# Kernel tuning notes

Hardware: AMD Instinct MI355X
Metric: run time of the kernel (lower is better)

Reference implementation:

```python
import jax, jax.numpy as jnp
import numpy as np
from jax import lax

K, N, DV, NBPS, NITER, BATCH = 1056, 2112, 5, 4, 20, 1024
M = N - K            # number of parity checks
E = M * (DV + 1)     # Tanner-graph edges (H = [A | I_m], row weight DV+1)
NSYM = N // NBPS     # QAM symbols per codeword


def _qam16():
    # Sionna-style Gray-mapped QAM constellation, unit average energy.
    def pam_gray(b):
        if len(b) > 1:
            return (1 - 2 * b[0]) * (2 ** (len(b) - 1) - pam_gray(b[1:]))
        return 1 - 2 * b[0]
    pts = []
    for i in range(2 ** NBPS):
        b = [(i >> (NBPS - 1 - j)) & 1 for j in range(NBPS)]
        pts.append(complex(pam_gray(b[0::2]), pam_gray(b[1::2])))
    pts = np.asarray(pts)
    pts = pts / np.sqrt(np.mean(np.abs(pts) ** 2))
    return pts.real.astype(np.float32), pts.imag.astype(np.float32)


def setup_inputs() -> dict:
    key = jax.random.key(0)
    rng = np.random.default_rng(0)
    bits = jnp.asarray(rng.integers(0, 2, size=(BATCH, K)), jnp.int32)
    # sparse A: DV distinct info-bit columns per check row
    a_idx = np.argsort(rng.random((M, K)), axis=1)[:, :DV].astype(np.int32)
    edge_vn = np.concatenate([a_idx, K + np.arange(M, dtype=np.int32)[:, None]], axis=1).reshape(-1)
    edge_cn = np.repeat(np.arange(M, dtype=np.int32), DV + 1)
    pre, pim = _qam16()
    k1, k2 = jax.random.split(key)
    return {
        "bits": bits,
        "a_idx": jnp.asarray(a_idx),
        "edge_cn": jnp.asarray(edge_cn),
        "edge_vn": jnp.asarray(edge_vn),
        "points_re": jnp.asarray(pre),
        "points_im": jnp.asarray(pim),
        "noise_re": jax.random.normal(k1, (BATCH, NSYM), jnp.float32),
        "noise_im": jax.random.normal(k2, (BATCH, NSYM), jnp.float32),
        "ebno_db": jnp.float32(4.0),
    }


def _forward(bits, a_idx, edge_cn, edge_vn, points_re, points_im, noise_re, noise_im, ebno_db):
    B = bits.shape[0]
    coderate = K / N
    # ebnodb2no (Es = 1): N0 = 1 / (EbN0_lin * coderate * bits_per_symbol)
    no = 1.0 / (10.0 ** (ebno_db / 10.0) * coderate * NBPS)
    # --- LDPC encode: H = [A | I], parity_i = XOR of info bits in row i ---
    parity = jnp.sum(bits[:, a_idx], axis=-1) % 2          # [B, M]
    cw = jnp.concatenate([bits, parity], axis=1)           # [B, N]
    # --- QAM map ---
    w = jnp.array([1 << (NBPS - 1 - j) for j in range(NBPS)], jnp.int32)
    sym = jnp.sum(cw.reshape(B, NSYM, NBPS) * w, axis=-1)  # [B, S]
    sigma = jnp.sqrt(no / 2.0)
    y_re = points_re[sym] + sigma * noise_re
    y_im = points_im[sym] + sigma * noise_im
    # --- APP demap: LLR = log p(b=0|y) - log p(b=1|y) ---
    d2 = (y_re[..., None] - points_re) ** 2 + (y_im[..., None] - points_im) ** 2  # [B,S,16]
    lg = (-d2 / no)[..., None]                                                     # [B,S,16,1]
    lab = (jnp.arange(2 ** NBPS)[:, None] >> jnp.arange(NBPS - 1, -1, -1)) & 1     # [16,4]
    NEG = jnp.float32(-1e30)
    l0 = jax.nn.logsumexp(jnp.where(lab == 0, lg, NEG), axis=2)
    l1 = jax.nn.logsumexp(jnp.where(lab == 1, lg, NEG), axis=2)
    llr = (l0 - l1).reshape(B, N)                          # [B, N]
    # --- sum-product BP, flooding schedule, NITER iterations ---
    def marg(c2v):  # scatter-add check->variable messages onto variable nodes
        return jnp.zeros((B, N), c2v.dtype).at[:, edge_vn].add(c2v)
    def step(c2v, _):
        v2c = (llr + marg(c2v))[:, edge_vn] - c2v          # extrinsic VN->CN [B,E]
        av = jnp.clip(jnp.abs(v2c), 1e-6, 20.0)
        lt = jnp.log(jnp.tanh(av * 0.5))                   # log|tanh(.)| <= 0
        sg = (v2c < 0).astype(v2c.dtype)
        cs = jnp.zeros((B, M), v2c.dtype).at[:, edge_cn].add(lt)
        ns = jnp.zeros((B, M), v2c.dtype).at[:, edge_cn].add(sg)
        ex = jnp.exp(jnp.minimum(cs[:, edge_cn] - lt, -1e-7))   # prod over other edges < 1
        sp = 1.0 - 2.0 * jnp.mod(ns[:, edge_cn] - sg, 2.0)      # sign product over other edges
        return sp * 2.0 * jnp.arctanh(ex), None
    c2v, _ = lax.scan(step, jnp.zeros((B, E), jnp.float32), None, length=NITER)
    tot = llr + marg(c2v)
    bits_rx = (tot[:, :K] < 0).astype(jnp.float32)         # hard_out=True
    return bits.astype(jnp.float32), bits_rx, tot[:, :K]


def reference(bits, a_idx, edge_cn, edge_vn, points_re, points_im, noise_re, noise_im, ebno_db):
    b, brx, _ = _forward(bits, a_idx, edge_cn, edge_vn, points_re, points_im,
                         noise_re, noise_im, ebno_db)
    return b, brx
```

## Files before the change

### kernel.cpp

```cpp
#include <hip/hip_runtime.h>

#define K_     1056
#define N_     2112
#define M_     1056
#define E_     6336
#define NIE_   5280
#define CAP_   6336
#define ALL_   7392
#define DV_    5
#define ROW_   6
#define NSYM_  528
#define NITER_ 20
#define BATCH_ 1024
#define BS_    1024
#define KMAX_  2

#define LOG2E_ 1.4426950408889634f
#define AVLO_  (1e-6f * LOG2E_)
#define AVHI_  (20.0f * LOG2E_)
#define QC_    0.99999988f

__device__ __forceinline__ int seg_stride(int d) { return d | 1; }

__device__ __forceinline__ float fexp2(float x) { return __builtin_amdgcn_exp2f(x); }
__device__ __forceinline__ float flog2(float x) { return __builtin_amdgcn_logf(x); }
__device__ __forceinline__ float frcp(float x)  { return __builtin_amdgcn_rcpf(x); }

__global__ __launch_bounds__(BS_, 8) void link_kernel(
    const int*   __restrict__ bits,
    const int*   __restrict__ a_idx,
    const float* __restrict__ points_re,
    const float* __restrict__ points_im,
    const float* __restrict__ noise_re,
    const float* __restrict__ noise_im,
    const float* __restrict__ ebno_db,
    const int*   __restrict__ edge_vn,
    float*       __restrict__ out)
{
#pragma clang fp contract(off)
    const int b   = blockIdx.x;
    const int tid = threadIdx.x;

    __shared__ float s_all[ALL_];
    __shared__ float s_pre[16];
    __shared__ float s_pim[16];
    __shared__ int   s_hist[32];
    __shared__ int   s_binStart[32];
    __shared__ int   s_binBase[32];

    float* s_mem  = s_all;
    float* s_marg = s_all + CAP_;

    int* sc        = (int*)(s_all + N_);
    int* s_deg     = sc;
    int* s_perm    = sc + K_;
    int* s_offslot = sc + 2 * K_;
    int* s_cnt     = sc + 3 * K_;

    if (tid < 16) {
        s_pre[tid] = points_re[tid];
        s_pim[tid] = points_im[tid];
    }
    if (tid < 32) s_hist[tid] = 0;

    const float eb    = ebno_db[0];
    const float no    = 1.0f / ((powf(10.0f, eb / 10.0f) * 0.5f) * 4.0f);
    const float sigma = sqrtf(no / 2.0f);

    for (int i = tid; i < K_; i += BS_) {
        int v = bits[b * K_ + i];
        s_mem[i] = (float)v;
        out[b * K_ + i] = (float)v;
    }
    __syncthreads();

    for (int m = tid; m < M_; m += BS_) {
        float acc = 0.0f;
        #pragma unroll
        for (int d = 0; d < DV_; ++d) acc += s_mem[a_idx[m * DV_ + d]];
        s_mem[K_ + m] = (float)(((int)acc) & 1);
    }
    for (int v = tid; v < K_; v += BS_) { s_deg[v] = 0; s_cnt[v] = 0; }
    __syncthreads();

    for (int s = tid; s < NSYM_; s += BS_) {
        int c0 = (int)s_mem[4 * s + 0];
        int c1 = (int)s_mem[4 * s + 1];
        int c2 = (int)s_mem[4 * s + 2];
        int c3 = (int)s_mem[4 * s + 3];
        int sym = c0 * 8 + c1 * 4 + c2 * 2 + c3;
        float yre = s_pre[sym] + sigma * noise_re[b * NSYM_ + s];
        float yim = s_pim[sym] + sigma * noise_im[b * NSYM_ + s];
        #pragma unroll
        for (int j = 0; j < 4; ++j) {
            float m0 = -1e30f, m1 = -1e30f;
            #pragma unroll
            for (int p = 0; p < 16; ++p) {
                float dre  = yre - s_pre[p];
                float dim_ = yim - s_pim[p];
                float lg   = -(dre * dre + dim_ * dim_) / no;
                if (((p >> (3 - j)) & 1) == 0) m0 = fmaxf(m0, lg);
                else                           m1 = fmaxf(m1, lg);
            }
            float sum0 = 0.0f, sum1 = 0.0f;
            #pragma unroll
            for (int p = 0; p < 16; ++p) {
                float dre  = yre - s_pre[p];
                float dim_ = yim - s_pim[p];
                float lg   = -(dre * dre + dim_ * dim_) / no;
                if (((p >> (3 - j)) & 1) == 0) sum0 += __expf(lg - m0);
                else                           sum1 += __expf(lg - m1);
            }
            float llr = (m0 + __logf(sum0)) - (m1 + __logf(sum1));
            s_mem[4 * s + j] = llr * LOG2E_;
        }
    }
    for (int idx = tid; idx < NIE_; idx += BS_) {
        int m = idx / 5, j = idx - m * 5;
        atomicAdd(&s_deg[edge_vn[m * ROW_ + j]], 1);
    }
    __syncthreads();

    for (int v = tid; v < K_; v += BS_) atomicAdd(&s_hist[s_deg[v] & 31], 1);
    __syncthreads();
    if (tid == 0) {
        int accS = 0, accB = 0;
        for (int d = 0; d < 32; ++d) {
            int c = s_hist[d];
            s_binStart[d] = accS;
            s_binBase[d]  = accB;
            s_hist[d]     = accS;
            accS += c;
            accB += c * seg_stride(d);
        }
    }
    __syncthreads();
    for (int v = tid; v < K_; v += BS_) {
        int d    = s_deg[v];
        int slot = atomicAdd(&s_hist[d & 31], 1);
        int base = s_binBase[d] + (slot - s_binStart[d]) * seg_stride(d);
        s_perm[slot]  = v | (d << 16);
        s_offslot[v]  = base | (slot << 16);
    }
    __syncthreads();

    int      pv[KMAX_];
    unsigned od[KMAX_];
    float    lr[KMAX_];
    #pragma unroll
    for (int k = 0; k < KMAX_; ++k) {
        int s = tid + BS_ * k;
        if (s < K_) {
            int w = s_perm[s];
            int v = w & 0xFFFF;
            int d = w >> 16;
            int base = s_binBase[d] + (s - s_binStart[d]) * seg_stride(d);
            pv[k] = v;
            od[k] = (unsigned)base | ((unsigned)d << 16);
            lr[k] = s_mem[v];
            s_marg[s] = lr[k];
        } else { pv[k] = 0; od[k] = 0; lr[k] = 0.0f; }
    }
    float    t5[KMAX_];
    unsigned vnp[KMAX_][5];
    float    c2v[KMAX_][5];
    #pragma unroll
    for (int kk = 0; kk < KMAX_; ++kk) {
        int m = tid + BS_ * kk;
        if (m < M_) {
            #pragma unroll
            for (int j = 0; j < 5; ++j) {
                int v = edge_vn[m * ROW_ + j];
                int r = atomicAdd(&s_cnt[v], 1);
                int w = s_offslot[v];
                int slot = w >> 16;
                int epos = (w & 0xFFFF) + r;
                vnp[kk][j] = (unsigned)(slot << 2) | ((unsigned)(epos << 2) << 16);
                c2v[kk][j] = 0.0f;
            }
            float lrP = s_mem[K_ + m];
            float av  = __builtin_amdgcn_fmed3f(fabsf(lrP), AVLO_, AVHI_);
            float e   = fexp2(-av);
            float tm  = (1.0f - e) * frcp(1.0f + e);
            t5[kk] = copysignf(tm, lrP);
        } else {
            t5[kk] = 0.0f;
            #pragma unroll
            for (int j = 0; j < 5; ++j) { vnp[kk][j] = 0; c2v[kk][j] = 0.0f; }
        }
    }
    __syncthreads();

    for (int it = 0; it < NITER_; ++it) {
        #pragma unroll
        for (int kk = 0; kk < KMAX_; ++kk) {
            int m = tid + BS_ * kk;
            if (m < M_) {
                float tj[5];
                #pragma unroll
                for (int j = 0; j < 5; ++j) {
                    unsigned w = vnp[kk][j];
                    float mgv = *(const float*)((const char*)s_all +
                                 ((w & 0xFFFFu) + (unsigned)(CAP_ * 4)));
                    float v2c = mgv - c2v[kk][j];
                    float av  = __builtin_amdgcn_fmed3f(fabsf(v2c), AVLO_, AVHI_);
                    float e   = fexp2(-av);
                    float tm  = (1.0f - e) * frcp(1.0f + e);
                    tj[j] = copysignf(tm, v2c);
                }
                float qv[5];
                float pr = t5[kk];
                #pragma unroll
                for (int j = 0; j < 5; ++j) { qv[j] = pr; pr *= tj[j]; }
                float sf = 1.0f;
                #pragma unroll
                for (int j = 4; j >= 0; --j) { qv[j] *= sf; sf *= tj[j]; }
                #pragma unroll
                for (int j = 0; j < 5; ++j) {
                    float q = __builtin_amdgcn_fmed3f(qv[j], -QC_, QC_);
                    float r = flog2((1.0f + q) * frcp(1.0f - q));
                    c2v[kk][j] = r;
                    *(float*)((char*)s_all + (vnp[kk][j] >> 16)) = r;
                }
            }
        }
        __syncthreads();
        #pragma unroll
        for (int k = 0; k < KMAX_; ++k) {
            int s = tid + BS_ * k;
            if (s < K_) {
                int base = (int)(od[k] & 0xFFFFu);
                int dg   = (int)(od[k] >> 16);
                float mg = lr[k];
                int d = 0;
                for (; d + 1 < dg; d += 2) {
                    mg += s_mem[base + d];
                    mg += s_mem[base + d + 1];
                }
                if (d < dg) mg += s_mem[base + d];
                s_marg[s] = mg;
                if (it == NITER_ - 1)
                    out[(size_t)BATCH_ * K_ + b * K_ + pv[k]] =
                        (mg < 0.0f) ? 1.0f : 0.0f;
            }
        }
        __syncthreads();
    }
}

extern "C" void kernel_launch(void* const* d_in, const int* in_sizes, int n_in,
                              void* d_out, int out_size, void* d_ws, size_t ws_size,
                              hipStream_t stream) {
    const int*   bits    = (const int*)  d_in[0];
    const int*   a_idx   = (const int*)  d_in[1];
    const int*   edge_vn = (const int*)  d_in[3];
    const float* pre     = (const float*)d_in[4];
    const float* pim     = (const float*)d_in[5];
    const float* nre     = (const float*)d_in[6];
    const float* nim     = (const float*)d_in[7];
    const float* ebno    = (const float*)d_in[8];

    link_kernel<<<BATCH_, BS_, 0, stream>>>(bits, a_idx, pre, pim, nre, nim,
                                            ebno, edge_vn, (float*)d_out);
}
```

Before: 181.5 us.

## Decode two codewords per block with interleaved float2 shared memory

Each block now processes two codewords. Messages and marginals are stored as interleaved float2 in shared memory, so the graph-structure setup (degree histogram, permutation, edge offsets) is amortized across both codewords and each LDS access moves 8 bytes. The grid is halved and shared memory usage doubles, which lowers occupancy and increases per-thread register pressure from the float2 arrays. An explicit zeroing pass over the message area is added before the iterations.

```diff
diff --git a/kernel.cpp b/kernel.cpp
--- a/kernel.cpp
+++ b/kernel.cpp
@@ -14,6 +14,7 @@
 #define BATCH_ 1024
 #define BS_    1024
 #define KMAX_  2
+#define NCW_   2
 
 #define LOG2E_ 1.4426950408889634f
 #define AVLO_  (1e-6f * LOG2E_)
@@ -38,20 +39,22 @@
     float*       __restrict__ out)
 {
 #pragma clang fp contract(off)
-    const int b   = blockIdx.x;
+    const int blk = blockIdx.x;
+    const int b0  = blk * NCW_;
+    const int b1  = b0 + 1;
     const int tid = threadIdx.x;
 
-    __shared__ float s_all[ALL_];
-    __shared__ float s_pre[16];
-    __shared__ float s_pim[16];
-    __shared__ int   s_hist[32];
-    __shared__ int   s_binStart[32];
-    __shared__ int   s_binBase[32];
-
-    float* s_mem  = s_all;
-    float* s_marg = s_all + CAP_;
-
-    int* sc        = (int*)(s_all + N_);
+    __shared__ float2 s_all2[ALL_];
+    __shared__ float  s_pre[16];
+    __shared__ float  s_pim[16];
+    __shared__ int    s_hist[32];
+    __shared__ int    s_binStart[32];
+    __shared__ int    s_binBase[32];
+
+    float* s_f = (float*)s_all2;
+    char*  sb  = (char*)s_all2;
+
+    int* sc        = (int*)(s_all2 + N_);
     int* s_deg     = sc;
     int* s_perm    = sc + K_;
     int* s_offslot = sc + 2 * K_;
@@ -68,29 +71,41 @@
     const float sigma = sqrtf(no / 2.0f);
 
     for (int i = tid; i < K_; i += BS_) {
-        int v = bits[b * K_ + i];
-        s_mem[i] = (float)v;
-        out[b * K_ + i] = (float)v;
+        int v0 = bits[b0 * K_ + i];
+        int v1 = bits[b1 * K_ + i];
+        s_f[2 * i + 0] = (float)v0;
+        s_f[2 * i + 1] = (float)v1;
+        out[b0 * K_ + i] = (float)v0;
+        out[b1 * K_ + i] = (float)v1;
     }
     __syncthreads();
 
     for (int m = tid; m < M_; m += BS_) {
-        float acc = 0.0f;
+        float ax = 0.0f, ay = 0.0f;
         #pragma unroll
-        for (int d = 0; d < DV_; ++d) acc += s_mem[a_idx[m * DV_ + d]];
-        s_mem[K_ + m] = (float)(((int)acc) & 1);
+        for (int d = 0; d < DV_; ++d) {
+            float2 f = s_all2[a_idx[m * DV_ + d]];
+            ax += f.x; ay += f.y;
+        }
+        float2 p;
+        p.x = (float)(((int)ax) & 1);
+        p.y = (float)(((int)ay) & 1);
+        s_all2[K_ + m] = p;
     }
     for (int v = tid; v < K_; v += BS_) { s_deg[v] = 0; s_cnt[v] = 0; }
     __syncthreads();
 
-    for (int s = tid; s < NSYM_; s += BS_) {
-        int c0 = (int)s_mem[4 * s + 0];
-        int c1 = (int)s_mem[4 * s + 1];
-        int c2 = (int)s_mem[4 * s + 2];
-        int c3 = (int)s_mem[4 * s + 3];
+    for (int tsk = tid; tsk < NCW_ * NSYM_; tsk += BS_) {
+        int cw = (tsk >= NSYM_) ? 1 : 0;
+        int s  = tsk - cw * NSYM_;
+        int bcw = b0 + cw;
+        int c0 = (int)s_f[2 * (4 * s + 0) + cw];
+        int c1 = (int)s_f[2 * (4 * s + 1) + cw];
+        int c2 = (int)s_f[2 * (4 * s + 2) + cw];
+        int c3 = (int)s_f[2 * (4 * s + 3) + cw];
         int sym = c0 * 8 + c1 * 4 + c2 * 2 + c3;
-        float yre = s_pre[sym] + sigma * noise_re[b * NSYM_ + s];
-        float yim = s_pim[sym] + sigma * noise_im[b * NSYM_ + s];
+        float yre = s_pre[sym] + sigma * noise_re[bcw * NSYM_ + s];
+        float yim = s_pim[sym] + sigma * noise_im[bcw * NSYM_ + s];
         #pragma unroll
         for (int j = 0; j < 4; ++j) {
             float m0 = -1e30f, m1 = -1e30f;
@@ -112,7 +127,7 @@
                 else                           sum1 += __expf(lg - m1);
             }
             float llr = (m0 + __logf(sum0)) - (m1 + __logf(sum1));
-            s_mem[4 * s + j] = llr * LOG2E_;
+            s_f[2 * (4 * s + j) + cw] = llr * LOG2E_;
         }
     }
     for (int idx = tid; idx < NIE_; idx += BS_) {
@@ -144,9 +159,8 @@
     }
     __syncthreads();
 
-    int      pv[KMAX_];
     unsigned od[KMAX_];
-    float    lr[KMAX_];
+    float2   lr[KMAX_];
     #pragma unroll
     for (int k = 0; k < KMAX_; ++k) {
         int s = tid + BS_ * k;
@@ -155,15 +169,14 @@
             int v = w & 0xFFFF;
             int d = w >> 16;
             int base = s_binBase[d] + (s - s_binStart[d]) * seg_stride(d);
-            pv[k] = v;
-            od[k] = (unsigned)base | ((unsigned)d << 16);
-            lr[k] = s_mem[v];
-            s_marg[s] = lr[k];
-        } else { pv[k] = 0; od[k] = 0; lr[k] = 0.0f; }
-    }
-    float    t5[KMAX_];
+            od[k] = (unsigned)base | ((unsigned)d << 13) | ((unsigned)v << 18);
+            lr[k] = s_all2[v];
+            s_all2[CAP_ + s] = lr[k];
+        } else { od[k] = 0; lr[k] = make_float2(0.0f, 0.0f); }
+    }
+    float2   t5[KMAX_];
     unsigned vnp[KMAX_][5];
-    float    c2v[KMAX_][5];
+    float2   c2v[KMAX_][5];
     #pragma unroll
     for (int kk = 0; kk < KMAX_; ++kk) {
         int m = tid + BS_ * kk;
@@ -175,20 +188,26 @@
                 int w = s_offslot[v];
                 int slot = w >> 16;
                 int epos = (w & 0xFFFF) + r;
-                vnp[kk][j] = (unsigned)(slot << 2) | ((unsigned)(epos << 2) << 16);
-                c2v[kk][j] = 0.0f;
-            }
-            float lrP = s_mem[K_ + m];
-            float av  = __builtin_amdgcn_fmed3f(fabsf(lrP), AVLO_, AVHI_);
-            float e   = fexp2(-av);
-            float tm  = (1.0f - e) * frcp(1.0f + e);
-            t5[kk] = copysignf(tm, lrP);
+                vnp[kk][j] = (unsigned)(slot << 3) | ((unsigned)(epos << 3) << 16);
+                c2v[kk][j] = make_float2(0.0f, 0.0f);
+            }
+            float2 lrP = s_all2[K_ + m];
+            float avx = __builtin_amdgcn_fmed3f(fabsf(lrP.x), AVLO_, AVHI_);
+            float avy = __builtin_amdgcn_fmed3f(fabsf(lrP.y), AVLO_, AVHI_);
+            float ex  = fexp2(-avx), ey = fexp2(-avy);
+            float tmx = (1.0f - ex) * frcp(1.0f + ex);
+            float tmy = (1.0f - ey) * frcp(1.0f + ey);
+            t5[kk] = make_float2(copysignf(tmx, lrP.x), copysignf(tmy, lrP.y));
         } else {
-            t5[kk] = 0.0f;
+            t5[kk] = make_float2(0.0f, 0.0f);
             #pragma unroll
-            for (int j = 0; j < 5; ++j) { vnp[kk][j] = 0; c2v[kk][j] = 0.0f; }
-        }
-    }
+            for (int j = 0; j < 5; ++j) {
+                vnp[kk][j] = 0; c2v[kk][j] = make_float2(0.0f, 0.0f);
+            }
+        }
+    }
+    __syncthreads();
+    for (int i = tid; i < CAP_; i += BS_) s_all2[i] = make_float2(0.0f, 0.0f);
     __syncthreads();
 
     for (int it = 0; it < NITER_; ++it) {
@@ -196,31 +215,43 @@
         for (int kk = 0; kk < KMAX_; ++kk) {
             int m = tid + BS_ * kk;
             if (m < M_) {
-                float tj[5];
+                float tjx[5], tjy[5];
                 #pragma unroll
                 for (int j = 0; j < 5; ++j) {
                     unsigned w = vnp[kk][j];
-                    float mgv = *(const float*)((const char*)s_all +
-                                 ((w & 0xFFFFu) + (unsigned)(CAP_ * 4)));
-                    float v2c = mgv - c2v[kk][j];
-                    float av  = __builtin_amdgcn_fmed3f(fabsf(v2c), AVLO_, AVHI_);
-                    float e   = fexp2(-av);
-                    float tm  = (1.0f - e) * frcp(1.0f + e);
-                    tj[j] = copysignf(tm, v2c);
-                }
-                float qv[5];
-                float pr = t5[kk];
-                #pragma unroll
-                for (int j = 0; j < 5; ++j) { qv[j] = pr; pr *= tj[j]; }
-                float sf = 1.0f;
-                #pragma unroll
-                for (int j = 4; j >= 0; --j) { qv[j] *= sf; sf *= tj[j]; }
+                    float2 mgv = *(const float2*)(sb +
+                                 ((w & 0xFFFFu) + (unsigned)(CAP_ * 8)));
+                    float vx = mgv.x - c2v[kk][j].x;
+                    float vy = mgv.y - c2v[kk][j].y;
+                    float avx = __builtin_amdgcn_fmed3f(fabsf(vx), AVLO_, AVHI_);
+                    float avy = __builtin_amdgcn_fmed3f(fabsf(vy), AVLO_, AVHI_);
+                    float ex = fexp2(-avx), ey = fexp2(-avy);
+                    float tmx = (1.0f - ex) * frcp(1.0f + ex);
+                    float tmy = (1.0f - ey) * frcp(1.0f + ey);
+                    tjx[j] = copysignf(tmx, vx);
+                    tjy[j] = copysignf(tmy, vy);
+                }
+                float qx[5], qy[5];
+                float prx = t5[kk].x, pry = t5[kk].y;
                 #pragma unroll
                 for (int j = 0; j < 5; ++j) {
-                    float q = __builtin_amdgcn_fmed3f(qv[j], -QC_, QC_);
-                    float r = flog2((1.0f + q) * frcp(1.0f - q));
-                    c2v[kk][j] = r;
-                    *(float*)((char*)s_all + (vnp[kk][j] >> 16)) = r;
+                    qx[j] = prx; qy[j] = pry;
+                    prx *= tjx[j]; pry *= tjy[j];
+                }
+                float sfx = 1.0f, sfy = 1.0f;
+                #pragma unroll
+                for (int j = 4; j >= 0; --j) {
+                    qx[j] *= sfx; qy[j] *= sfy;
+                    sfx *= tjx[j]; sfy *= tjy[j];
+                }
+                #pragma unroll
+                for (int j = 0; j < 5; ++j) {
+                    float qcx = __builtin_amdgcn_fmed3f(qx[j], -QC_, QC_);
+                    float qcy = __builtin_amdgcn_fmed3f(qy[j], -QC_, QC_);
+                    float rx = flog2((1.0f + qcx) * frcp(1.0f - qcx));
+                    float ry = flog2((1.0f + qcy) * frcp(1.0f - qcy));
+                    c2v[kk][j] = make_float2(rx, ry);
+                    *(float2*)(sb + (vnp[kk][j] >> 16)) = c2v[kk][j];
                 }
             }
         }
@@ -229,19 +260,26 @@
         for (int k = 0; k < KMAX_; ++k) {
             int s = tid + BS_ * k;
             if (s < K_) {
-                int base = (int)(od[k] & 0xFFFFu);
-                int dg   = (int)(od[k] >> 16);
-                float mg = lr[k];
+                int base = (int)(od[k] & 0x1FFFu);
+                int dg   = (int)((od[k] >> 13) & 31u);
+                float mgx = lr[k].x, mgy = lr[k].y;
                 int d = 0;
                 for (; d + 1 < dg; d += 2) {
-                    mg += s_mem[base + d];
-                    mg += s_mem[base + d + 1];
-                }
-                if (d < dg) mg += s_mem[base + d];
-                s_marg[s] = mg;
-                if (it == NITER_ - 1)
-                    out[(size_t)BATCH_ * K_ + b * K_ + pv[k]] =
-                        (mg < 0.0f) ? 1.0f : 0.0f;
+                    float2 f0 = s_all2[base + d];
+                    float2 f1 = s_all2[base + d + 1];
+                    mgx += f0.x; mgy += f0.y;
+                    mgx += f1.x; mgy += f1.y;
+                }
+                if (d < dg) {
+                    float2 f0 = s_all2[base + d];
+                    mgx += f0.x; mgy += f0.y;
+                }
+                s_all2[CAP_ + s] = make_float2(mgx, mgy);
+                if (it == NITER_ - 1) {
+                    int pv = (int)(od[k] >> 18);
+                    out[(size_t)BATCH_ * K_ + b0 * K_ + pv] = (mgx < 0.0f) ? 1.0f : 0.0f;
+                    out[(size_t)BATCH_ * K_ + b1 * K_ + pv] = (mgy < 0.0f) ? 1.0f : 0.0f;
+                }
             }
         }
         __syncthreads();
@@ -260,6 +298,6 @@
     const float* nim     = (const float*)d_in[7];
     const float* ebno    = (const float*)d_in[8];
 
-    link_kernel<<<BATCH_, BS_, 0, stream>>>(bits, a_idx, pre, pim, nre, nim,
-                                            ebno, edge_vn, (float*)d_out);
+    link_kernel<<<BATCH_ / NCW_, BS_, 0, stream>>>(bits, a_idx, pre, pim, nre, nim,
+                                                   ebno, edge_vn, (float*)d_out);
 }
```

Measured after the change: 177.8 us. 1.02x faster.
